# Performance work log

Hardware: AMD Instinct MI355X
Metric: run time of the kernel (lower is better)

The kernel has to match this reference:

```python
import jax, jax.numpy as jnp
import numpy as np

R = 16
ALPHA = 32
SCALING = ALPHA / R  # 2.0


def setup_inputs() -> dict:
    key = jax.random.key(0)
    k_x, k_w, k_b, k_a, k_bm = jax.random.split(key, 5)
    d = 1024
    x = jax.random.normal(k_x, (4, 4096, d), dtype=jnp.float32)
    W = jax.random.normal(k_w, (d, d), dtype=jnp.float32) * 0.02
    b = jax.random.normal(k_b, (d,), dtype=jnp.float32) * 0.02
    A = jax.random.normal(k_a, (R, d), dtype=jnp.float32) * 0.02
    B = jax.random.normal(k_bm, (d, R), dtype=jnp.float32) * 0.02
    return {"x": x, "W": W, "b": b, "A": A, "B": B}


def reference(x, W, b, A, B):
    # base linear: x @ W^T + b   (W: [out, in])
    base = jnp.einsum("bsd,od->bso", x, W) + b
    # low-rank update: (x @ A^T) @ B^T, scaled (dropout p=0 -> identity)
    u = jnp.einsum("bsd,rd->bsr", x, A)   # [B, S, r]
    update = jnp.einsum("bsr,or->bso", u, B)
    return base + SCALING * update
```

## Files before the change

### kernel.cpp

```cpp
#include <hip/hip_runtime.h>


typedef __bf16 bf16x8 __attribute__((ext_vector_type(8)));
typedef float f32x4 __attribute__((ext_vector_type(4)));
typedef unsigned short ushort8 __attribute__((ext_vector_type(8)));

__device__ __forceinline__ unsigned short f2bf(float f) {
    __bf16 h = (__bf16)f;
    union { __bf16 b; unsigned short u; } v; v.b = h; return v.u;
}
__device__ __forceinline__ ushort8 cvt8(f32x4 a, f32x4 b) {
    ushort8 o;
#pragma unroll
    for (int i = 0; i < 4; ++i) { o[i] = f2bf(a[i]); o[i + 4] = f2bf(b[i]); }
    return o;
}
__device__ __forceinline__ void gld16(const unsigned short* g, unsigned short* l) {
    __builtin_amdgcn_global_load_lds(
        (const __attribute__((address_space(1))) unsigned int*)g,
        (__attribute__((address_space(3))) unsigned int*)l, 16, 0, 0);
}

#define FENCE() asm volatile("" ::: "memory")
#define BARRIER() do { FENCE(); __builtin_amdgcn_s_barrier(); FENCE(); } while (0)

__global__ __launch_bounds__(256) void prep(
    const float* __restrict__ W, const float* __restrict__ A,
    const float* __restrict__ B, unsigned short* __restrict__ Weff)
{
    const int idx = blockIdx.x * 256 + threadIdx.x;
    const int o  = idx >> 7;
    const int kc = (idx & 127) << 3;
    float br[16];
#pragma unroll
    for (int r = 0; r < 16; ++r) br[r] = 2.0f * B[o * 16 + r];
    float acc[8];
    const float* wrow = W + (size_t)o * 1024 + kc;
#pragma unroll
    for (int j = 0; j < 8; ++j) acc[j] = wrow[j];
#pragma unroll
    for (int r = 0; r < 16; ++r) {
        const float* arow = A + r * 1024 + kc;
#pragma unroll
        for (int j = 0; j < 8; ++j) acc[j] += br[r] * arow[j];
    }
    ushort8 o8;
#pragma unroll
    for (int j = 0; j < 8; ++j) o8[j] = f2bf(acc[j]);
    *(ushort8*)(Weff + (size_t)o * 1024 + kc) = o8;
}

#define PHASE_MFMA(LO)                                              \
    do { BARRIER();                                                 \
         asm volatile("s_waitcnt lgkmcnt(0)" ::: "memory");         \
         __builtin_amdgcn_sched_barrier(0);            \
         __builtin_amdgcn_s_setprio(1);                             \
         _Pragma("unroll")                                          \
         for (int m2 = 0; m2 < 4; ++m2)                             \
             _Pragma("unroll")                                      \
             for (int n2 = 0; n2 < 2; ++n2)                         \
                 acc[(LO) + m2][n2] = __builtin_amdgcn_mfma_f32_16x16x32_bf16( \
                     fa[(LO) + m2], fb[n2], acc[(LO) + m2][n2], 0, 0, 0);      \
         __builtin_amdgcn_s_setprio(0);                             \
         BARRIER(); } while (0)

__global__ __launch_bounds__(512, 4) void gemm256(
    const float* __restrict__ Xf,
    const unsigned short* __restrict__ Wt,
    const float* __restrict__ bias,
    float* __restrict__ out)
{
    extern __shared__ __align__(16) unsigned short lds[];

    const int t    = threadIdx.x;
    const int lane = t & 63;
    const int w    = t >> 6;
    const int wr   = w >> 2;
    const int wc   = w & 3;
    const int r16  = lane & 15;
    const int quad = lane >> 4;

    const int nwg = gridDim.x;
    int swz = blockIdx.x;
    if ((nwg & 7) == 0) swz = (swz & 7) * (nwg >> 3) + (swz >> 3);
    const int bm = (swz >> 3) * 256;
    const int bn = (swz & 7) * 128;

    const int r  = t >> 2;
    const int c  = t & 3;
    const int xr = c ^ ((r >> 1) & 3);
    const float* gA0 = Xf + (size_t)(bm + r) * 1024 + c * 8;
    const float* gA1 = gA0 + 131072;
    const unsigned short* pB = Wt + (size_t)(bn + r) * 1024 + xr * 8;
    const int wd = r * 32 + xr * 8;
    const int lc = t * 8;

    const int sw = (quad ^ ((r16 >> 1) & 3)) * 8;
    const int aB = wr * 512 + r16 * 32 + sw;
    const int bB = wc * 512 + r16 * 32 + sw;

    f32x4 acc[8][2];
#pragma unroll
    for (int i = 0; i < 8; ++i)
#pragma unroll
        for (int jj = 0; jj < 2; ++jj)
            acc[i][jj] = (f32x4){0.f, 0.f, 0.f, 0.f};

    f32x4 sA[4];

    sA[0] = *(const f32x4*)(gA0);      sA[1] = *(const f32x4*)(gA0 + 4);
    sA[2] = *(const f32x4*)(gA1);      sA[3] = *(const f32x4*)(gA1 + 4);
    FENCE();
    gld16(pB, lds + 8192 + lc);        FENCE();
    *(ushort8*)(lds + wd)        = cvt8(sA[0], sA[1]);
    *(ushort8*)(lds + 4096 + wd) = cvt8(sA[2], sA[3]);
    sA[0] = *(const f32x4*)(gA0 + 32); sA[1] = *(const f32x4*)(gA0 + 36);
    sA[2] = *(const f32x4*)(gA1 + 32); sA[3] = *(const f32x4*)(gA1 + 36);
    FENCE();
    gld16(pB + 32, lds + 12288 + 8192 + lc);
    asm volatile("s_waitcnt vmcnt(5)" ::: "memory");
    asm volatile("s_waitcnt lgkmcnt(0)" ::: "memory");
    BARRIER();

#pragma unroll 2
    for (int j = 0; j < 32; ++j) {
        const int cur = (j & 1) * 12288;
        const int nxt = cur ^ 12288;
        const unsigned short* Lb = lds + cur;
        const int k2 = (j + 2) * 32;

        bf16x8 fa[8], fb[2];

        if (j < 31) {
            *(ushort8*)(lds + nxt + wd)        = cvt8(sA[0], sA[1]);
            *(ushort8*)(lds + nxt + 4096 + wd) = cvt8(sA[2], sA[3]);
        }
#pragma unroll
        for (int mt = 0; mt < 4; ++mt)
            fa[mt] = *(const bf16x8*)(Lb + mt * 1024 + aB);
#pragma unroll
        for (int nt = 0; nt < 2; ++nt)
            fb[nt] = *(const bf16x8*)(Lb + 8192 + nt * 2048 + bB);
        PHASE_MFMA(0);

#pragma unroll
        for (int mt = 4; mt < 8; ++mt)
            fa[mt] = *(const bf16x8*)(Lb + 4096 + (mt - 4) * 1024 + aB);
        if (j < 30) {
            sA[0] = *(const f32x4*)(gA0 + k2);      sA[1] = *(const f32x4*)(gA0 + k2 + 4);
            sA[2] = *(const f32x4*)(gA1 + k2);      sA[3] = *(const f32x4*)(gA1 + k2 + 4);
            FENCE();
            gld16(pB + k2, lds + cur + 8192 + lc);
            FENCE();
        }
        if (j < 30)       asm volatile("s_waitcnt vmcnt(5)" ::: "memory");
        else if (j == 30) asm volatile("s_waitcnt vmcnt(0)" ::: "memory");
        PHASE_MFMA(4);
    }

    const int orow0 = bm + wr * 16 + quad * 4;
    const int ocol0 = bn + wc * 16 + r16;
#pragma unroll
    for (int nt = 0; nt < 2; ++nt) {
        const float bv = bias[ocol0 + nt * 64];
#pragma unroll
        for (int mt = 0; mt < 8; ++mt) {
            float* orow = out + (size_t)(orow0 + mt * 32) * 1024 + (ocol0 + nt * 64);
#pragma unroll
            for (int i = 0; i < 4; ++i)
                orow[(size_t)i * 1024] = acc[mt][nt][i] + bv;
        }
    }
}

template <bool XF32>
__global__ __launch_bounds__(256) void gemm_bt(
    const void* __restrict__ X_, const unsigned short* __restrict__ Wt,
    const float* __restrict__ bias, float* __restrict__ out)
{
    __shared__ __align__(16) unsigned short lA[128 * 32];
    __shared__ __align__(16) unsigned short lB[128 * 32];

    const int t    = threadIdx.x;
    const int lane = t & 63;
    const int w    = t >> 6;
    const int bm   = blockIdx.x * 128;
    const int bn   = blockIdx.y * 128;
    const int wm   = (w & 1) * 64;
    const int wn   = (w >> 1) * 64;
    const int r16  = lane & 15;
    const int quad = lane >> 4;

    const int srow = t >> 2;
    const int gc   = (t & 3) ^ ((srow >> 1) & 3);
    unsigned short* lsA = lA + t * 8;
    unsigned short* lsB = lB + t * 8;
    const size_t ga0 = (size_t)(bm + srow) * 1024 + gc * 8;
    const size_t ga1 = (size_t)(bm + srow + 64) * 1024 + gc * 8;
    const unsigned short* gB0 = Wt + (size_t)(bn + srow) * 1024 + gc * 8;

    const int p    = (quad ^ ((r16 >> 1) & 3)) * 8;
    const int aoff = (wm + r16) * 32 + p;
    const int boff = (wn + r16) * 32 + p;

    const unsigned short* Xb = (const unsigned short*)X_;
    const float*          Xf = (const float*)X_;

    f32x4 acc[4][4];
#pragma unroll
    for (int i = 0; i < 4; ++i)
#pragma unroll
        for (int j = 0; j < 4; ++j) {
            f32x4 z = {0.f, 0.f, 0.f, 0.f};
            acc[i][j] = z;
        }

    for (int kt = 0; kt < 1024; kt += 32) {
        if (XF32) {
            f32x4 a0 = *(const f32x4*)(Xf + ga0 + kt);
            f32x4 a1 = *(const f32x4*)(Xf + ga0 + kt + 4);
            f32x4 a2 = *(const f32x4*)(Xf + ga1 + kt);
            f32x4 a3 = *(const f32x4*)(Xf + ga1 + kt + 4);
            *(ushort8*)lsA          = cvt8(a0, a1);
            *(ushort8*)(lsA + 2048) = cvt8(a2, a3);
        } else {
            gld16(Xb + ga0 + kt, lsA);
            gld16(Xb + ga1 + kt, lsA + 2048);
        }
        gld16(gB0 + kt,             lsB);
        gld16(gB0 + kt + 64 * 1024, lsB + 2048);
        __syncthreads();

        bf16x8 fa[4], fb[4];
#pragma unroll
        for (int mt = 0; mt < 4; ++mt) fa[mt] = *(const bf16x8*)(lA + aoff + mt * 16 * 32);
#pragma unroll
        for (int nt = 0; nt < 4; ++nt) fb[nt] = *(const bf16x8*)(lB + boff + nt * 16 * 32);

#pragma unroll
        for (int mt = 0; mt < 4; ++mt)
#pragma unroll
            for (int nt = 0; nt < 4; ++nt)
                acc[mt][nt] = __builtin_amdgcn_mfma_f32_16x16x32_bf16(
                    fa[mt], fb[nt], acc[mt][nt], 0, 0, 0);

        __syncthreads();
    }

    const int orow0 = bm + wm + quad * 4;
    const int ocol0 = bn + wn + r16;
#pragma unroll
    for (int nt = 0; nt < 4; ++nt) {
        const float bv = bias[ocol0 + nt * 16];
#pragma unroll
        for (int mt = 0; mt < 4; ++mt)
#pragma unroll
            for (int i = 0; i < 4; ++i)
                out[(size_t)(orow0 + mt * 16 + i) * 1024 + (ocol0 + nt * 16)] =
                    acc[mt][nt][i] + bv;
    }
}

extern "C" void kernel_launch(void* const* d_in, const int* in_sizes, int n_in,
                              void* d_out, int out_size, void* d_ws, size_t ws_size,
                              hipStream_t stream) {
    const float* x  = (const float*)d_in[0];
    const float* W  = (const float*)d_in[1];
    const float* b  = (const float*)d_in[2];
    const float* A  = (const float*)d_in[3];
    const float* Bm = (const float*)d_in[4];
    float* out = (float*)d_out;

    const int M = in_sizes[0] / 1024;

    const bool fast = (ws_size >= (2u << 20) + 4096) && (M % 256 == 0);
    unsigned short* Weff = (unsigned short*)d_ws;
    hipLaunchKernelGGL(prep, dim3(512), dim3(256), 0, stream, W, A, Bm, Weff);
    if (fast) {
        hipLaunchKernelGGL(gemm256, dim3((M / 256) * 8), dim3(512), 49152, stream,
                           x, Weff, b, out);
    } else {
        hipLaunchKernelGGL((gemm_bt<true>), dim3(M / 128, 8), dim3(256), 0, stream,
                           (const void*)x, Weff, b, out);
    }
}
```

Measured before the change: 179.7 us.

## Deepen fp32 A-operand prefetch with two register sets in GEMM main loop

Restructures the K loop into explicit even/odd halves, each with its own register set for the fp32 X tile, so global loads of A are issued two K-steps ahead instead of one. This hides more global-load latency behind the MFMA phases. The cost is extra VGPRs for the second staging set, which could pressure occupancy at the launch bound of 4 waves, plus more intricate vmcnt accounting.

Measured after the change: 220.0 us. 1.22x slower.

```diff
diff --git a/kernel.cpp b/kernel.cpp
--- a/kernel.cpp
+++ b/kernel.cpp
@@ -64,6 +64,16 @@
          __builtin_amdgcn_s_setprio(0);                             \
          BARRIER(); } while (0)
 
+#define LOADA(S, KT)                                                           \
+    do { S[0] = *(const f32x4*)(gA0 + (KT)); S[1] = *(const f32x4*)(gA0 + (KT) + 4); \
+         S[2] = *(const f32x4*)(gA1 + (KT)); S[3] = *(const f32x4*)(gA1 + (KT) + 4); \
+         FENCE(); } while (0)
+
+#define PUBA(S, BUF)                                                           \
+    do { *(ushort8*)(lds + (BUF) + wd)        = cvt8(S[0], S[1]);              \
+         *(ushort8*)(lds + (BUF) + 4096 + wd) = cvt8(S[2], S[3]);              \
+         FENCE(); } while (0)
+
 __global__ __launch_bounds__(512, 4) void gemm256(
     const float* __restrict__ Xf,
     const unsigned short* __restrict__ Wt,
@@ -106,56 +116,62 @@
         for (int jj = 0; jj < 2; ++jj)
             acc[i][jj] = (f32x4){0.f, 0.f, 0.f, 0.f};
 
-    f32x4 sA[4];
-
-    sA[0] = *(const f32x4*)(gA0);      sA[1] = *(const f32x4*)(gA0 + 4);
-    sA[2] = *(const f32x4*)(gA1);      sA[3] = *(const f32x4*)(gA1 + 4);
-    FENCE();
-    gld16(pB, lds + 8192 + lc);        FENCE();
-    *(ushort8*)(lds + wd)        = cvt8(sA[0], sA[1]);
-    *(ushort8*)(lds + 4096 + wd) = cvt8(sA[2], sA[3]);
-    sA[0] = *(const f32x4*)(gA0 + 32); sA[1] = *(const f32x4*)(gA0 + 36);
-    sA[2] = *(const f32x4*)(gA1 + 32); sA[3] = *(const f32x4*)(gA1 + 36);
-    FENCE();
-    gld16(pB + 32, lds + 12288 + 8192 + lc);
-    asm volatile("s_waitcnt vmcnt(5)" ::: "memory");
+    f32x4 sEV[4], sOD[4];
+
+    LOADA(sEV, 0);
+    gld16(pB, lds + 8192 + lc);           FENCE();
+    PUBA(sEV, 0);
+    LOADA(sEV, 32);
+    gld16(pB + 32, lds + 12288 + 8192 + lc); FENCE();
+    LOADA(sOD, 64);
+    asm volatile("s_waitcnt vmcnt(9)" ::: "memory");
     asm volatile("s_waitcnt lgkmcnt(0)" ::: "memory");
     BARRIER();
 
-#pragma unroll 2
-    for (int j = 0; j < 32; ++j) {
-        const int cur = (j & 1) * 12288;
-        const int nxt = cur ^ 12288;
-        const unsigned short* Lb = lds + cur;
-        const int k2 = (j + 2) * 32;
-
-        bf16x8 fa[8], fb[2];
-
-        if (j < 31) {
-            *(ushort8*)(lds + nxt + wd)        = cvt8(sA[0], sA[1]);
-            *(ushort8*)(lds + nxt + 4096 + wd) = cvt8(sA[2], sA[3]);
-        }
-#pragma unroll
-        for (int mt = 0; mt < 4; ++mt)
-            fa[mt] = *(const bf16x8*)(Lb + mt * 1024 + aB);
-#pragma unroll
-        for (int nt = 0; nt < 2; ++nt)
-            fb[nt] = *(const bf16x8*)(Lb + 8192 + nt * 2048 + bB);
-        PHASE_MFMA(0);
-
-#pragma unroll
-        for (int mt = 4; mt < 8; ++mt)
-            fa[mt] = *(const bf16x8*)(Lb + 4096 + (mt - 4) * 1024 + aB);
-        if (j < 30) {
-            sA[0] = *(const f32x4*)(gA0 + k2);      sA[1] = *(const f32x4*)(gA0 + k2 + 4);
-            sA[2] = *(const f32x4*)(gA1 + k2);      sA[3] = *(const f32x4*)(gA1 + k2 + 4);
-            FENCE();
-            gld16(pB + k2, lds + cur + 8192 + lc);
-            FENCE();
-        }
-        if (j < 30)       asm volatile("s_waitcnt vmcnt(5)" ::: "memory");
-        else if (j == 30) asm volatile("s_waitcnt vmcnt(0)" ::: "memory");
-        PHASE_MFMA(4);
+    for (int i = 0; i < 16; ++i) {
+        {
+            bf16x8 fa[8], fb[2];
+            PUBA(sEV, 12288);
+#pragma unroll
+            for (int mt = 0; mt < 4; ++mt)
+                fa[mt] = *(const bf16x8*)(lds + mt * 1024 + aB);
+#pragma unroll
+            for (int nt = 0; nt < 2; ++nt)
+                fb[nt] = *(const bf16x8*)(lds + 8192 + nt * 2048 + bB);
+            PHASE_MFMA(0);
+#pragma unroll
+            for (int mt = 4; mt < 8; ++mt)
+                fa[mt] = *(const bf16x8*)(lds + 4096 + (mt - 4) * 1024 + aB);
+            if (i <= 14) {
+                LOADA(sEV, (2 * i + 3) * 32);
+                gld16(pB + (2 * i + 2) * 32, lds + 8192 + lc);
+                FENCE();
+                asm volatile("s_waitcnt vmcnt(5)" ::: "memory");
+            } else {
+                asm volatile("s_waitcnt vmcnt(0)" ::: "memory");
+            }
+            PHASE_MFMA(4);
+        }
+        {
+            bf16x8 fa[8], fb[2];
+            if (i <= 14) PUBA(sOD, 0);
+#pragma unroll
+            for (int mt = 0; mt < 4; ++mt)
+                fa[mt] = *(const bf16x8*)(lds + 12288 + mt * 1024 + aB);
+#pragma unroll
+            for (int nt = 0; nt < 2; ++nt)
+                fb[nt] = *(const bf16x8*)(lds + 12288 + 8192 + nt * 2048 + bB);
+            PHASE_MFMA(0);
+#pragma unroll
+            for (int mt = 4; mt < 8; ++mt)
+                fa[mt] = *(const bf16x8*)(lds + 12288 + 4096 + (mt - 4) * 1024 + aB);
+            if (i <= 13) LOADA(sOD, (2 * i + 4) * 32);
+            if (i <= 14) { gld16(pB + (2 * i + 3) * 32, lds + 12288 + 8192 + lc);
+                           FENCE(); }
+            if (i <= 13)      asm volatile("s_waitcnt vmcnt(5)" ::: "memory");
+            else if (i == 14) asm volatile("s_waitcnt vmcnt(1)" ::: "memory");
+            PHASE_MFMA(4);
+        }
     }
 
     const int orow0 = bm + wr * 16 + quad * 4;
```

## Stage fp32 X tiles directly into LDS and convert to bf16 at fragment load

Applied to the files above, without the earlier changes.

The X tile is now copied as fp32 straight into LDS with async global_load_lds, using an XOR swizzle, instead of being loaded into registers, converted to bf16 and written to LDS. The conversion to bf16 moves to after the LDS fragment read, just before the MFMAs. The wave-to-tile mapping also changes to a 4x4 accumulator layout with four B fragments reused per A fragment, and the LDS footprint grows to 80 KB for double buffering. This removes VGPR staging and conversion from the load path, but doubles LDS traffic for A and may lower occupancy.

Result: no change. 178.9 us (-0.5%).

```diff
diff --git a/kernel.cpp b/kernel.cpp
--- a/kernel.cpp
+++ b/kernel.cpp
@@ -9,13 +9,16 @@
     __bf16 h = (__bf16)f;
     union { __bf16 b; unsigned short u; } v; v.b = h; return v.u;
 }
-__device__ __forceinline__ ushort8 cvt8(f32x4 a, f32x4 b) {
+__device__ __forceinline__ ushort8 cvt8u(f32x4 a, f32x4 b) {
     ushort8 o;
 #pragma unroll
     for (int i = 0; i < 4; ++i) { o[i] = f2bf(a[i]); o[i + 4] = f2bf(b[i]); }
     return o;
 }
-__device__ __forceinline__ void gld16(const unsigned short* g, unsigned short* l) {
+__device__ __forceinline__ bf16x8 cvt8(f32x4 a, f32x4 b) {
+    union { ushort8 u; bf16x8 h; } v; v.u = cvt8u(a, b); return v.h;
+}
+__device__ __forceinline__ void gld16(const void* g, void* l) {
     __builtin_amdgcn_global_load_lds(
         (const __attribute__((address_space(1))) unsigned int*)g,
         (__attribute__((address_space(3))) unsigned int*)l, 16, 0, 0);
@@ -50,33 +53,19 @@
     *(ushort8*)(Weff + (size_t)o * 1024 + kc) = o8;
 }
 
-#define PHASE_MFMA(LO)                                              \
-    do { BARRIER();                                                 \
-         asm volatile("s_waitcnt lgkmcnt(0)" ::: "memory");         \
-         __builtin_amdgcn_sched_barrier(0);            \
-         __builtin_amdgcn_s_setprio(1);                             \
-         _Pragma("unroll")                                          \
-         for (int m2 = 0; m2 < 4; ++m2)                             \
-             _Pragma("unroll")                                      \
-             for (int n2 = 0; n2 < 2; ++n2)                         \
-                 acc[(LO) + m2][n2] = __builtin_amdgcn_mfma_f32_16x16x32_bf16( \
-                     fa[(LO) + m2], fb[n2], acc[(LO) + m2][n2], 0, 0, 0);      \
-         __builtin_amdgcn_s_setprio(0);                             \
-         BARRIER(); } while (0)
-
 __global__ __launch_bounds__(512, 4) void gemm256(
     const float* __restrict__ Xf,
     const unsigned short* __restrict__ Wt,
     const float* __restrict__ bias,
     float* __restrict__ out)
 {
-    extern __shared__ __align__(16) unsigned short lds[];
+    extern __shared__ __align__(16) char lds[];
 
     const int t    = threadIdx.x;
     const int lane = t & 63;
     const int w    = t >> 6;
-    const int wr   = w >> 2;
-    const int wc   = w & 3;
+    const int wr   = w & 3;
+    const int wc   = w >> 2;
     const int r16  = lane & 15;
     const int quad = lane >> 4;
 
@@ -86,86 +75,106 @@
     const int bm = (swz >> 3) * 256;
     const int bn = (swz & 7) * 128;
 
-    const int r  = t >> 2;
-    const int c  = t & 3;
-    const int xr = c ^ ((r >> 1) & 3);
-    const float* gA0 = Xf + (size_t)(bm + r) * 1024 + c * 8;
-    const float* gA1 = gA0 + 131072;
-    const unsigned short* pB = Wt + (size_t)(bn + r) * 1024 + xr * 8;
-    const int wd = r * 32 + xr * 8;
-    const int lc = t * 8;
-
-    const int sw = (quad ^ ((r16 >> 1) & 3)) * 8;
-    const int aB = wr * 512 + r16 * 32 + sw;
-    const int bB = wc * 512 + r16 * 32 + sw;
-
-    f32x4 acc[8][2];
-#pragma unroll
-    for (int i = 0; i < 8; ++i)
-#pragma unroll
-        for (int jj = 0; jj < 2; ++jj)
+    const int ar = t >> 3;
+    const int ac = (t & 7) ^ (ar & 7);
+    const float* gA = Xf + (size_t)(bm + ar) * 1024 + ac * 4;
+    const int adst = t * 16;
+
+    const int brw = t >> 2;
+    const int bcc = (t & 3) ^ ((brw >> 1) & 3);
+    const unsigned short* pB = Wt + (size_t)(bn + brw) * 1024 + bcc * 8;
+    const int bdst = 32768 + t * 16;
+
+    const int o0  = ((2 * quad) ^ (r16 & 7)) * 16;
+    const int o1  = ((2 * quad + 1) ^ (r16 & 7)) * 16;
+    const int hA0 = (wr * 16 + r16) * 128;
+    const int hA1 = ((4 + wr) * 16 + r16) * 128;
+    const int bB0 = 32768 + (wc * 16 + r16) * 64 + (quad ^ ((r16 >> 1) & 3)) * 16;
+
+    f32x4 acc[4][4];
+#pragma unroll
+    for (int i = 0; i < 4; ++i)
+#pragma unroll
+        for (int jj = 0; jj < 4; ++jj)
             acc[i][jj] = (f32x4){0.f, 0.f, 0.f, 0.f};
 
-    f32x4 sA[4];
-
-    sA[0] = *(const f32x4*)(gA0);      sA[1] = *(const f32x4*)(gA0 + 4);
-    sA[2] = *(const f32x4*)(gA1);      sA[3] = *(const f32x4*)(gA1 + 4);
-    FENCE();
-    gld16(pB, lds + 8192 + lc);        FENCE();
-    *(ushort8*)(lds + wd)        = cvt8(sA[0], sA[1]);
-    *(ushort8*)(lds + 4096 + wd) = cvt8(sA[2], sA[3]);
-    sA[0] = *(const f32x4*)(gA0 + 32); sA[1] = *(const f32x4*)(gA0 + 36);
-    sA[2] = *(const f32x4*)(gA1 + 32); sA[3] = *(const f32x4*)(gA1 + 36);
-    FENCE();
-    gld16(pB + 32, lds + 12288 + 8192 + lc);
-    asm volatile("s_waitcnt vmcnt(5)" ::: "memory");
-    asm volatile("s_waitcnt lgkmcnt(0)" ::: "memory");
+#define STAGE_A(HALF, BUF, K)                                                     \
+    do { gld16(gA + (HALF) * 131072 + (K),         lds + (BUF) + (HALF) * 16384 + adst);        \
+         gld16(gA + (HALF) * 131072 + 65536 + (K), lds + (BUF) + (HALF) * 16384 + 8192 + adst); \
+         FENCE(); } while (0)
+#define STAGE_B(BUF, K)                                                           \
+    do { gld16(pB + (K), lds + (BUF) + bdst); FENCE(); } while (0)
+
+    STAGE_A(0, 0, 0);
+    STAGE_B(0, 0);
+    STAGE_A(1, 0, 0);
+    STAGE_A(0, 40960, 32);
+    STAGE_B(40960, 32);
+    asm volatile("s_waitcnt vmcnt(3)" ::: "memory");
     BARRIER();
 
 #pragma unroll 2
     for (int j = 0; j < 32; ++j) {
-        const int cur = (j & 1) * 12288;
-        const int nxt = cur ^ 12288;
-        const unsigned short* Lb = lds + cur;
-        const int k2 = (j + 2) * 32;
-
-        bf16x8 fa[8], fb[2];
-
-        if (j < 31) {
-            *(ushort8*)(lds + nxt + wd)        = cvt8(sA[0], sA[1]);
-            *(ushort8*)(lds + nxt + 4096 + wd) = cvt8(sA[2], sA[3]);
-        }
-#pragma unroll
-        for (int mt = 0; mt < 4; ++mt)
-            fa[mt] = *(const bf16x8*)(Lb + mt * 1024 + aB);
-#pragma unroll
-        for (int nt = 0; nt < 2; ++nt)
-            fb[nt] = *(const bf16x8*)(Lb + 8192 + nt * 2048 + bB);
-        PHASE_MFMA(0);
-
-#pragma unroll
-        for (int mt = 4; mt < 8; ++mt)
-            fa[mt] = *(const bf16x8*)(Lb + 4096 + (mt - 4) * 1024 + aB);
-        if (j < 30) {
-            sA[0] = *(const f32x4*)(gA0 + k2);      sA[1] = *(const f32x4*)(gA0 + k2 + 4);
-            sA[2] = *(const f32x4*)(gA1 + k2);      sA[3] = *(const f32x4*)(gA1 + k2 + 4);
-            FENCE();
-            gld16(pB + k2, lds + cur + 8192 + lc);
-            FENCE();
-        }
-        if (j < 30)       asm volatile("s_waitcnt vmcnt(5)" ::: "memory");
+        const int cur = (j & 1) * 40960;
+        const int nxt = cur ^ 40960;
+
+        f32x4 a0l = *(const f32x4*)(lds + cur + hA0 + o0);
+        f32x4 a0h = *(const f32x4*)(lds + cur + hA0 + o1);
+        f32x4 a1l = *(const f32x4*)(lds + cur + hA1 + o0);
+        f32x4 a1h = *(const f32x4*)(lds + cur + hA1 + o1);
+        bf16x8 fb[4];
+#pragma unroll
+        for (int nt = 0; nt < 4; ++nt)
+            fb[nt] = *(const bf16x8*)(lds + cur + bB0 + nt * 2048);
+        if (j < 31) STAGE_A(1, nxt, (j + 1) * 32);
+        BARRIER();
+        asm volatile("s_waitcnt lgkmcnt(0)" ::: "memory");
+        __builtin_amdgcn_sched_barrier(0);
+        __builtin_amdgcn_s_setprio(1);
+        {
+            bf16x8 fa0 = cvt8(a0l, a0h), fa1 = cvt8(a1l, a1h);
+#pragma unroll
+            for (int nt = 0; nt < 4; ++nt) {
+                acc[0][nt] = __builtin_amdgcn_mfma_f32_16x16x32_bf16(fa0, fb[nt], acc[0][nt], 0, 0, 0);
+                acc[1][nt] = __builtin_amdgcn_mfma_f32_16x16x32_bf16(fa1, fb[nt], acc[1][nt], 0, 0, 0);
+            }
+        }
+        __builtin_amdgcn_s_setprio(0);
+        BARRIER();
+
+        f32x4 a2l = *(const f32x4*)(lds + cur + 16384 + hA0 + o0);
+        f32x4 a2h = *(const f32x4*)(lds + cur + 16384 + hA0 + o1);
+        f32x4 a3l = *(const f32x4*)(lds + cur + 16384 + hA1 + o0);
+        f32x4 a3h = *(const f32x4*)(lds + cur + 16384 + hA1 + o1);
+        if (j < 30) { STAGE_A(0, cur, (j + 2) * 32); STAGE_B(cur, (j + 2) * 32); }
+        if (j < 30)       asm volatile("s_waitcnt vmcnt(3)" ::: "memory");
         else if (j == 30) asm volatile("s_waitcnt vmcnt(0)" ::: "memory");
-        PHASE_MFMA(4);
-    }
+        BARRIER();
+        asm volatile("s_waitcnt lgkmcnt(0)" ::: "memory");
+        __builtin_amdgcn_sched_barrier(0);
+        __builtin_amdgcn_s_setprio(1);
+        {
+            bf16x8 fa2 = cvt8(a2l, a2h), fa3 = cvt8(a3l, a3h);
+#pragma unroll
+            for (int nt = 0; nt < 4; ++nt) {
+                acc[2][nt] = __builtin_amdgcn_mfma_f32_16x16x32_bf16(fa2, fb[nt], acc[2][nt], 0, 0, 0);
+                acc[3][nt] = __builtin_amdgcn_mfma_f32_16x16x32_bf16(fa3, fb[nt], acc[3][nt], 0, 0, 0);
+            }
+        }
+        __builtin_amdgcn_s_setprio(0);
+        BARRIER();
+    }
+#undef STAGE_A
+#undef STAGE_B
 
     const int orow0 = bm + wr * 16 + quad * 4;
     const int ocol0 = bn + wc * 16 + r16;
 #pragma unroll
-    for (int nt = 0; nt < 2; ++nt) {
-        const float bv = bias[ocol0 + nt * 64];
-#pragma unroll
-        for (int mt = 0; mt < 8; ++mt) {
-            float* orow = out + (size_t)(orow0 + mt * 32) * 1024 + (ocol0 + nt * 64);
+    for (int nt = 0; nt < 4; ++nt) {
+        const float bv = bias[ocol0 + nt * 32];
+#pragma unroll
+        for (int mt = 0; mt < 4; ++mt) {
+            float* orow = out + (size_t)(orow0 + mt * 64) * 1024 + (ocol0 + nt * 32);
 #pragma unroll
             for (int i = 0; i < 4; ++i)
                 orow[(size_t)i * 1024] = acc[mt][nt][i] + bv;
@@ -221,8 +230,8 @@
             f32x4 a1 = *(const f32x4*)(Xf + ga0 + kt + 4);
             f32x4 a2 = *(const f32x4*)(Xf + ga1 + kt);
             f32x4 a3 = *(const f32x4*)(Xf + ga1 + kt + 4);
-            *(ushort8*)lsA          = cvt8(a0, a1);
-            *(ushort8*)(lsA + 2048) = cvt8(a2, a3);
+            *(ushort8*)lsA          = cvt8u(a0, a1);
+            *(ushort8*)(lsA + 2048) = cvt8u(a2, a3);
         } else {
             gld16(Xb + ga0 + kt, lsA);
             gld16(Xb + ga1 + kt, lsA + 2048);
@@ -277,7 +286,7 @@
     unsigned short* Weff = (unsigned short*)d_ws;
     hipLaunchKernelGGL(prep, dim3(512), dim3(256), 0, stream, W, A, Bm, Weff);
     if (fast) {
-        hipLaunchKernelGGL(gemm256, dim3((M / 256) * 8), dim3(512), 49152, stream,
+        hipLaunchKernelGGL(gemm256, dim3((M / 256) * 8), dim3(512), 81920, stream,
                            x, Weff, b, out);
     } else {
         hipLaunchKernelGGL((gemm_bt<true>), dim3(M / 128, 8), dim3(256), 0, stream,
```
